# Optimization experiments

Measured on AMD Instinct MI355X. Metric: run time of the kernel, lower is better.

Reference implementation:

```python
import jax, jax.numpy as jnp
import numpy as np

K = 16

def _local_cov(points):
    # points: [B, N, 3]. FoldingNet-style local covariance feature.
    xx = jnp.sum(points * points, axis=-1)                       # [B,N]
    inner = jnp.einsum('bnd,bmd->bnm', points, points)           # [B,N,N]
    pd = -xx[:, :, None] + 2.0 * inner - xx[:, None, :]          # negative sq dist
    _, idx = jax.lax.top_k(pd, K)                                # [B,N,K] nearest first (self at 0)
    n0 = jnp.take_along_axis(points, idx[:, :, 0][:, :, None], axis=1)  # [B,N,3]
    n1 = jnp.take_along_axis(points, idx[:, :, 1][:, :, None], axis=1)  # [B,N,3]
    cov = n0[..., :, None] * n1[..., None, :]                    # [B,N,3,3] outer product
    B, N = points.shape[0], points.shape[1]
    return jnp.concatenate([points, cov.reshape(B, N, 9)], axis=-1)     # [B,N,12]

def _stage(x, w1, b1, wr, br, w2, b2):
    h = jax.nn.relu(x @ w1 + b1)
    h = jax.nn.relu(h + (h @ wr + br))   # ResidualLinearLayer then ReLU
    return h @ w2 + b2                   # [B,N,1]

def setup_inputs() -> dict:
    key = jax.random.key(0)
    ks = jax.random.split(key, 16)
    B, N, F = 8, 4096, 512
    s = 0.02
    d = {
        'latent': jax.random.normal(ks[0], (B, N, F), jnp.float32),
        'reconstructed_points': jax.random.normal(ks[1], (B, 3, N), jnp.float32),
        's1_w1': jax.random.normal(ks[2], (F + 12, F), jnp.float32) * s,
        's1_b1': jnp.zeros((F,), jnp.float32),
        's1_wr': jax.random.normal(ks[3], (F, F), jnp.float32) * s,
        's1_br': jnp.zeros((F,), jnp.float32),
        's1_w2': jax.random.normal(ks[4], (F, 1), jnp.float32) * s,
        's1_b2': jnp.zeros((1,), jnp.float32),
        's2_w1': jax.random.normal(ks[5], (F + 1, F), jnp.float32) * s,
        's2_b1': jnp.zeros((F,), jnp.float32),
        's2_wr': jax.random.normal(ks[6], (F, F), jnp.float32) * s,
        's2_br': jnp.zeros((F,), jnp.float32),
        's2_w2': jax.random.normal(ks[7], (F, 1), jnp.float32) * s,
        's2_b2': jnp.zeros((1,), jnp.float32),
        's3_w1': jax.random.normal(ks[8], (F + 1, F), jnp.float32) * s,
        's3_b1': jnp.zeros((F,), jnp.float32),
        's3_wr': jax.random.normal(ks[9], (F, F), jnp.float32) * s,
        's3_br': jnp.zeros((F,), jnp.float32),
        's3_w2': jax.random.normal(ks[10], (F, 1), jnp.float32) * s,
        's3_b2': jnp.zeros((1,), jnp.float32),
    }
    return d

def reference(latent, reconstructed_points,
              s1_w1, s1_b1, s1_wr, s1_br, s1_w2, s1_b2,
              s2_w1, s2_b1, s2_wr, s2_br, s2_w2, s2_b2,
              s3_w1, s3_b1, s3_wr, s3_br, s3_w2, s3_b2):
    pts = jnp.transpose(reconstructed_points, (0, 2, 1))   # [B,N,3]
    local = _local_cov(pts)                                 # [B,N,12]
    f1 = jnp.concatenate([latent, local], axis=-1)
    std1 = _stage(f1, s1_w1, s1_b1, s1_wr, s1_br, s1_w2, s1_b2)
    f2 = jnp.concatenate([latent, std1], axis=-1)
    std2 = std1 + _stage(f2, s2_w1, s2_b1, s2_wr, s2_br, s2_w2, s2_b2)
    f3 = jnp.concatenate([latent, std2], axis=-1)
    std3 = std2 + _stage(f3, s3_w1, s3_b1, s3_wr, s3_br, s3_w2, s3_b2)
    return std3   # [B,N,1]
```

## Files before the change

### kernel.cpp

```cpp
#include <hip/hip_runtime.h>

typedef __bf16 bf16x8 __attribute__((ext_vector_type(8)));
typedef float f32x4 __attribute__((ext_vector_type(4)));

__device__ __forceinline__ unsigned short f2bf(float f) {
  unsigned u = __float_as_uint(f);
  u += 0x7FFFu + ((u >> 16) & 1u);
  return (unsigned short)(u >> 16);
}

__device__ __forceinline__ void gload_lds16(const void* g, void* l) {
  __builtin_amdgcn_global_load_lds((const __attribute__((address_space(1))) void*)g,
                                   (__attribute__((address_space(3))) void*)l,
                                   16, 0, 0);
}

#define NPTS 4096
#define LDX 576

__global__ __launch_bounds__(256) void convw6_kernel(
    const float* w0, const float* w1, const float* w2,
    const float* r0, const float* r1, const float* r2,
    unsigned short* d0, unsigned short* d1, unsigned short* d2,
    unsigned short* e0, unsigned short* e1, unsigned short* e2) {
  int z = blockIdx.z;
  const float* src; unsigned short* dst; int Ksrc, Kpad, addI;
  switch (z) {
    case 0: src = w0; dst = d0; Ksrc = 524; Kpad = 576; addI = 0; break;
    case 1: src = w1; dst = d1; Ksrc = 513; Kpad = 576; addI = 0; break;
    case 2: src = w2; dst = d2; Ksrc = 513; Kpad = 576; addI = 0; break;
    case 3: src = r0; dst = e0; Ksrc = 512; Kpad = 512; addI = 1; break;
    case 4: src = r1; dst = e1; Ksrc = 512; Kpad = 512; addI = 1; break;
    default: src = r2; dst = e2; Ksrc = 512; Kpad = 512; addI = 1; break;
  }
  int k0 = blockIdx.x * 32;
  if (k0 >= Kpad) return;
  __shared__ float tile[32][33];
  int n0 = blockIdx.y * 32;
  int tx = threadIdx.x & 31, ty = threadIdx.x >> 5;
#pragma unroll
  for (int r = 0; r < 32; r += 8) {
    int k = k0 + ty + r, n = n0 + tx;
    tile[ty + r][tx] = (k < Ksrc) ? src[(size_t)k * 512 + n] : 0.f;
  }
  __syncthreads();
#pragma unroll
  for (int r = 0; r < 32; r += 8) {
    int n = n0 + ty + r, k = k0 + tx;
    float v = tile[tx][ty + r];
    if (addI && n == k) v += 1.0f;
    dst[(size_t)n * Kpad + k] = f2bf(v);
  }
}

__global__ __launch_bounds__(256) void conv_latent_kernel(const float* __restrict__ latent,
                                                          unsigned short* __restrict__ X) {
  size_t idx = (size_t)blockIdx.x * 256 + threadIdx.x;
  size_t m = idx >> 7;
  int c4 = (int)(idx & 127) * 4;
  float4 v = *(const float4*)(latent + m * 512 + c4);
  ushort4 o;
  o.x = f2bf(v.x); o.y = f2bf(v.y); o.z = f2bf(v.z); o.w = f2bf(v.w);
  *(ushort4*)(X + m * LDX + c4) = o;
}

__device__ __forceinline__ void merge2(float& v1, int& i1, float& v2, int& i2, int mk) {
  float ov1 = __shfl_xor(v1, mk); int oi1 = __shfl_xor(i1, mk);
  float ov2 = __shfl_xor(v2, mk); int oi2 = __shfl_xor(i2, mk);
  bool ofirst = (ov1 > v1) || (ov1 == v1 && oi1 < i1);
  float n1v, n2v; int n1i, n2i;
  if (ofirst) {
    n1v = ov1; n1i = oi1;
    bool t = (v1 > ov2) || (v1 == ov2 && i1 < oi2);
    n2v = t ? v1 : ov2; n2i = t ? i1 : oi2;
  } else {
    n1v = v1; n1i = i1;
    bool t = (ov1 > v2) || (ov1 == v2 && oi1 < i2);
    n2v = t ? ov1 : v2; n2i = t ? oi1 : i2;
  }
  v1 = n1v; i1 = n1i; v2 = n2v; i2 = n2i;
}

__global__ __launch_bounds__(512) void knn_kernel(const float* __restrict__ rp,
                                                  unsigned short* __restrict__ X) {
  __shared__ float4 P[NPTS];
  int b = blockIdx.y;
  const float* base = rp + (size_t)b * 3 * NPTS;
  for (int j = threadIdx.x; j < NPTS; j += 512) {
    float x = base[j], y = base[NPTS + j], z = base[2 * NPTS + j];
    float xx = __fadd_rn(__fadd_rn(__fmul_rn(x, x), __fmul_rn(y, y)), __fmul_rn(z, z));
    P[j] = make_float4(x, y, z, xx);
  }
  __syncthreads();
  int wave = threadIdx.x >> 6, lane = threadIdx.x & 63;
  int grp = lane >> 4, slice = lane & 15;
  int il0 = wave * 16 + grp * 4;
  int ibase = blockIdx.x * 128 + il0;
  float tx[4], ty[4], tz[4], tc[4];
  float v1[4], v2[4]; int i1[4], i2[4];
#pragma unroll
  for (int p = 0; p < 4; ++p) {
    float4 pp = P[ibase + p];
    tx[p] = 2.f * pp.x; ty[p] = 2.f * pp.y; tz[p] = 2.f * pp.z; tc[p] = -pp.w;
    v1[p] = -3.4e38f; v2[p] = -3.4e38f; i1[p] = 0x7fffffff; i2[p] = 0x7fffffff;
  }
#pragma unroll 4
  for (int t = 0; t < NPTS / 16; ++t) {
    int j = t * 16 + slice;
    float4 pj = P[j];
#pragma unroll
    for (int p = 0; p < 4; ++p) {
      float d = __builtin_fmaf(tx[p], pj.x,
                __builtin_fmaf(ty[p], pj.y,
                __builtin_fmaf(tz[p], pj.z, tc[p]))) - pj.w;
      bool c1 = d > v1[p];
      bool c2 = d > v2[p];
      i2[p] = c1 ? i1[p] : (c2 ? j : i2[p]);
      v2[p] = __builtin_amdgcn_fmed3f(d, v1[p], v2[p]);
      i1[p] = c1 ? j : i1[p];
      v1[p] = fmaxf(v1[p], d);
    }
  }
#pragma unroll
  for (int mk = 1; mk <= 8; mk <<= 1)
#pragma unroll
    for (int p = 0; p < 4; ++p)
      merge2(v1[p], i1[p], v2[p], i2[p], mk);
  if (slice == 0) {
#pragma unroll
    for (int p = 0; p < 4; ++p) {
      float4 p0 = P[i1[p]];
      float4 p1 = P[i2[p]];
      size_t row = (size_t)b * NPTS + ibase + p;
      unsigned short* xp = X + row * LDX + 512;
      float px = 0.5f * tx[p], py = 0.5f * ty[p], pz = 0.5f * tz[p];
      float vals[12] = { px, py, pz,
                         p0.x * p1.x, p0.x * p1.y, p0.x * p1.z,
                         p0.y * p1.x, p0.y * p1.y, p0.y * p1.z,
                         p0.z * p1.x, p0.z * p1.y, p0.z * p1.z };
#pragma unroll
      for (int k = 0; k < 12; ++k) xp[k] = f2bf(vals[k]);
#pragma unroll
      for (int k = 12; k < 32; ++k) xp[k] = 0;
    }
  }
}

#define BM 128
#define BN 128
#define BK 64
__global__ __launch_bounds__(256) void gemm_relu_kernel(
    const unsigned short* __restrict__ Xb, const unsigned short* __restrict__ Wt,
    const float* __restrict__ bias, unsigned short* __restrict__ H,
    int K, int ldx, int ldw) {
  __shared__ unsigned short As[BM * BK];
  __shared__ unsigned short Bs[BN * BK];
  const int t = threadIdx.x;
  const int wave = t >> 6, lane = t & 63;
  const int m0 = blockIdx.y * BM, n0 = blockIdx.x * BN;
  const int wm = (wave >> 1) * 64, wn = (wave & 1) * 64;
  const int sr = lane >> 2;
  const int sc = (lane & 3) * 8;
  const int q = lane >> 4, lm = lane & 15;
  f32x4 acc[4][4] = {};
  for (int kt = 0; kt < K; kt += BK) {
#pragma unroll
    for (int r = 0; r < 2; ++r) {
      int c = r * 4 + wave;
#pragma unroll
      for (int h = 0; h < 2; ++h) {
        gload_lds16(Xb + (size_t)(m0 + c * 16 + sr) * ldx + kt + h * 32 + sc,
                    As + c * 1024 + h * 512);
        gload_lds16(Wt + (size_t)(n0 + c * 16 + sr) * ldw + kt + h * 32 + sc,
                    Bs + c * 1024 + h * 512);
      }
    }
    __syncthreads();
#pragma unroll
    for (int ks = 0; ks < 2; ++ks) {
      bf16x8 a[4], bb[4];
#pragma unroll
      for (int i = 0; i < 4; ++i)
        a[i] = *(const bf16x8*)(As + ((wm >> 4) + i) * 1024 + ks * 512 + lm * 32 + q * 8);
#pragma unroll
      for (int j = 0; j < 4; ++j)
        bb[j] = *(const bf16x8*)(Bs + ((wn >> 4) + j) * 1024 + ks * 512 + lm * 32 + q * 8);
#pragma unroll
      for (int i = 0; i < 4; ++i)
#pragma unroll
        for (int j = 0; j < 4; ++j)
          acc[i][j] = __builtin_amdgcn_mfma_f32_16x16x32_bf16(a[i], bb[j], acc[i][j], 0, 0, 0);
    }
    __syncthreads();
  }
#pragma unroll
  for (int i = 0; i < 4; ++i)
#pragma unroll
    for (int j = 0; j < 4; ++j) {
      int col = n0 + wn + j * 16 + lm;
      float bv = bias[col];
#pragma unroll
      for (int rg = 0; rg < 4; ++rg) {
        int row = m0 + wm + i * 16 + q * 4 + rg;
        float v = acc[i][j][rg] + bv;
        v = v > 0.f ? v : 0.f;
        H[(size_t)row * 512 + col] = f2bf(v);
      }
    }
}

__global__ __launch_bounds__(256) void gemm_res_kernel(
    const unsigned short* __restrict__ H1, const unsigned short* __restrict__ Wt,
    const float* __restrict__ br, const float* __restrict__ w2,
    float* __restrict__ so) {
  __shared__ unsigned short As[BM * BK];
  __shared__ unsigned short Bs[BN * BK];
  const int t = threadIdx.x;
  const int wave = t >> 6, lane = t & 63;
  const int m0 = blockIdx.y * BM, n0 = blockIdx.x * BN;
  const int wm = (wave >> 1) * 64, wn = (wave & 1) * 64;
  const int sr = lane >> 2, sc = (lane & 3) * 8;
  const int q = lane >> 4, lm = lane & 15;
  f32x4 acc[4][4] = {};
  for (int kt = 0; kt < 512; kt += BK) {
#pragma unroll
    for (int r = 0; r < 2; ++r) {
      int c = r * 4 + wave;
#pragma unroll
      for (int h = 0; h < 2; ++h) {
        gload_lds16(H1 + (size_t)(m0 + c * 16 + sr) * 512 + kt + h * 32 + sc,
                    As + c * 1024 + h * 512);
        gload_lds16(Wt + (size_t)(n0 + c * 16 + sr) * 512 + kt + h * 32 + sc,
                    Bs + c * 1024 + h * 512);
      }
    }
    __syncthreads();
#pragma unroll
    for (int ks = 0; ks < 2; ++ks) {
      bf16x8 a[4], bb[4];
#pragma unroll
      for (int i = 0; i < 4; ++i)
        a[i] = *(const bf16x8*)(As + ((wm >> 4) + i) * 1024 + ks * 512 + lm * 32 + q * 8);
#pragma unroll
      for (int j = 0; j < 4; ++j)
        bb[j] = *(const bf16x8*)(Bs + ((wn >> 4) + j) * 1024 + ks * 512 + lm * 32 + q * 8);
#pragma unroll
      for (int i = 0; i < 4; ++i)
#pragma unroll
        for (int j = 0; j < 4; ++j)
          acc[i][j] = __builtin_amdgcn_mfma_f32_16x16x32_bf16(a[i], bb[j], acc[i][j], 0, 0, 0);
    }
    __syncthreads();
  }
  float partial[4][4];
#pragma unroll
  for (int i = 0; i < 4; ++i)
#pragma unroll
    for (int rg = 0; rg < 4; ++rg) partial[i][rg] = 0.f;
#pragma unroll
  for (int i = 0; i < 4; ++i)
#pragma unroll
    for (int j = 0; j < 4; ++j) {
      int col = n0 + wn + j * 16 + lm;
      float bv = br[col], wv = w2[col];
#pragma unroll
      for (int rg = 0; rg < 4; ++rg) {
        float v = acc[i][j][rg] + bv;
        v = v > 0.f ? v : 0.f;
        partial[i][rg] += v * wv;
      }
    }
#pragma unroll
  for (int i = 0; i < 4; ++i)
#pragma unroll
    for (int rg = 0; rg < 4; ++rg) {
      float s = partial[i][rg];
      s += __shfl_xor(s, 1); s += __shfl_xor(s, 2);
      s += __shfl_xor(s, 4); s += __shfl_xor(s, 8);
      if (lm == 0) atomicAdd(&so[m0 + wm + i * 16 + q * 4 + rg], s);
    }
}

__global__ __launch_bounds__(256) void init_so_kernel(float* so, const float* b2) {
  int m = blockIdx.x * 256 + threadIdx.x;
  so[m] = b2[0];
}
__global__ __launch_bounds__(256) void update_kernel(float* std_cum, float* so,
                                                     unsigned short* X,
                                                     const float* b2_next, int first) {
  int m = blockIdx.x * 256 + threadIdx.x;
  float s = so[m];
  if (!first) s += std_cum[m];
  std_cum[m] = s;
  unsigned short* xp = X + (size_t)m * LDX + 512;
  xp[0] = f2bf(s);
#pragma unroll
  for (int k = 1; k < 12; ++k) xp[k] = 0;
  so[m] = b2_next[0];
}
__global__ __launch_bounds__(256) void finalize_kernel(float* out, const float* std_cum,
                                                       const float* so) {
  int m = blockIdx.x * 256 + threadIdx.x;
  out[m] = std_cum[m] + so[m];
}

extern "C" void kernel_launch(void* const* d_in, const int* in_sizes, int n_in,
                              void* d_out, int out_size, void* d_ws, size_t ws_size,
                              hipStream_t stream) {
  const int B = 8, N = NPTS, M = B * N;
  const float* latent = (const float*)d_in[0];
  const float* rp = (const float*)d_in[1];
  const float* w1[3] = {(const float*)d_in[2], (const float*)d_in[8], (const float*)d_in[14]};
  const float* b1[3] = {(const float*)d_in[3], (const float*)d_in[9], (const float*)d_in[15]};
  const float* wr[3] = {(const float*)d_in[4], (const float*)d_in[10], (const float*)d_in[16]};
  const float* br[3] = {(const float*)d_in[5], (const float*)d_in[11], (const float*)d_in[17]};
  const float* w2[3] = {(const float*)d_in[6], (const float*)d_in[12], (const float*)d_in[18]};
  const float* b2[3] = {(const float*)d_in[7], (const float*)d_in[13], (const float*)d_in[19]};

  char* ws = (char*)d_ws;
  auto carve = [&](size_t bytes) {
    char* p = ws;
    ws += (bytes + 255) & ~(size_t)255;
    return p;
  };
  unsigned short* X  = (unsigned short*)carve((size_t)M * LDX * 2);
  unsigned short* H1 = (unsigned short*)carve((size_t)M * 512 * 2);
  unsigned short* W1t[3], *Wrt[3];
  for (int s = 0; s < 3; ++s) W1t[s] = (unsigned short*)carve((size_t)512 * LDX * 2);
  for (int s = 0; s < 3; ++s) Wrt[s] = (unsigned short*)carve((size_t)512 * 512 * 2);
  float* std_cum = (float*)carve((size_t)M * 4);
  float* so      = (float*)carve((size_t)M * 4);

  convw6_kernel<<<dim3(LDX / 32, 16, 6), 256, 0, stream>>>(
      w1[0], w1[1], w1[2], wr[0], wr[1], wr[2],
      W1t[0], W1t[1], W1t[2], Wrt[0], Wrt[1], Wrt[2]);
  conv_latent_kernel<<<(M * 128) / 256, 256, 0, stream>>>(latent, X);
  knn_kernel<<<dim3(N / 128, B), 512, 0, stream>>>(rp, X);
  init_so_kernel<<<M / 256, 256, 0, stream>>>(so, b2[0]);

  for (int s = 0; s < 3; ++s) {
    gemm_relu_kernel<<<dim3(4, M / BM), 256, 0, stream>>>(X, W1t[s], b1[s], H1, LDX, LDX, LDX);
    gemm_res_kernel<<<dim3(4, M / BM), 256, 0, stream>>>(H1, Wrt[s], br[s], w2[s], so);
    if (s < 2)
      update_kernel<<<M / 256, 256, 0, stream>>>(std_cum, so, X, b2[s + 1], s == 0 ? 1 : 0);
  }
  finalize_kernel<<<M / 256, 256, 0, stream>>>((float*)d_out, std_cum, so);
}
```

Before: 400.0 us.

## Use 32x32 MFMA tiles in GEMMs and simplify kNN to nearest non-self

```diff
diff --git a/kernel.cpp b/kernel.cpp
--- a/kernel.cpp
+++ b/kernel.cpp
@@ -1,7 +1,7 @@
 #include <hip/hip_runtime.h>
 
 typedef __bf16 bf16x8 __attribute__((ext_vector_type(8)));
-typedef float f32x4 __attribute__((ext_vector_type(4)));
+typedef float f32x16 __attribute__((ext_vector_type(16)));
 
 __device__ __forceinline__ unsigned short f2bf(float f) {
   unsigned u = __float_as_uint(f);
@@ -64,21 +64,10 @@
   *(ushort4*)(X + m * LDX + c4) = o;
 }
 
-__device__ __forceinline__ void merge2(float& v1, int& i1, float& v2, int& i2, int mk) {
-  float ov1 = __shfl_xor(v1, mk); int oi1 = __shfl_xor(i1, mk);
-  float ov2 = __shfl_xor(v2, mk); int oi2 = __shfl_xor(i2, mk);
-  bool ofirst = (ov1 > v1) || (ov1 == v1 && oi1 < i1);
-  float n1v, n2v; int n1i, n2i;
-  if (ofirst) {
-    n1v = ov1; n1i = oi1;
-    bool t = (v1 > ov2) || (v1 == ov2 && i1 < oi2);
-    n2v = t ? v1 : ov2; n2i = t ? i1 : oi2;
-  } else {
-    n1v = v1; n1i = i1;
-    bool t = (ov1 > v2) || (ov1 == v2 && oi1 < i2);
-    n2v = t ? ov1 : v2; n2i = t ? oi1 : i2;
-  }
-  v1 = n1v; i1 = n1i; v2 = n2v; i2 = n2i;
+__device__ __forceinline__ void merge1(float& v, int& j, int mk) {
+  float ov = __shfl_xor(v, mk); int oj = __shfl_xor(j, mk);
+  bool take = (ov > v) || (ov == v && oj < j);
+  v = take ? ov : v; j = take ? oj : j;
 }
 
 __global__ __launch_bounds__(512) void knn_kernel(const float* __restrict__ rp,
@@ -89,55 +78,51 @@
   for (int j = threadIdx.x; j < NPTS; j += 512) {
     float x = base[j], y = base[NPTS + j], z = base[2 * NPTS + j];
     float xx = __fadd_rn(__fadd_rn(__fmul_rn(x, x), __fmul_rn(y, y)), __fmul_rn(z, z));
-    P[j] = make_float4(x, y, z, xx);
+    P[j] = make_float4(x, y, z, -xx);
   }
   __syncthreads();
   int wave = threadIdx.x >> 6, lane = threadIdx.x & 63;
   int grp = lane >> 4, slice = lane & 15;
-  int il0 = wave * 16 + grp * 4;
-  int ibase = blockIdx.x * 128 + il0;
-  float tx[4], ty[4], tz[4], tc[4];
-  float v1[4], v2[4]; int i1[4], i2[4];
-#pragma unroll
-  for (int p = 0; p < 4; ++p) {
-    float4 pp = P[ibase + p];
-    tx[p] = 2.f * pp.x; ty[p] = 2.f * pp.y; tz[p] = 2.f * pp.z; tc[p] = -pp.w;
-    v1[p] = -3.4e38f; v2[p] = -3.4e38f; i1[p] = 0x7fffffff; i2[p] = 0x7fffffff;
-  }
-#pragma unroll 4
+  int il0 = wave * 8 + grp * 2;
+  int ia = blockIdx.x * 64 + il0;
+  int ib = ia + 1;
+  float4 pa = P[ia], pb = P[ib];
+  float ax = 2.f * pa.x, ay = 2.f * pa.y, az = 2.f * pa.z;
+  float bx = 2.f * pb.x, by = 2.f * pb.y, bz = 2.f * pb.z;
+  float va = -3.4e38f, vb = -3.4e38f;
+  int ta = 0, tb = 0;
+  int sta = ((ia & 15) == slice) ? (ia >> 4) : -1;
+  int stb = ((ib & 15) == slice) ? (ib >> 4) : -1;
+  const float4* pp = P + slice;
+#pragma unroll 8
   for (int t = 0; t < NPTS / 16; ++t) {
-    int j = t * 16 + slice;
-    float4 pj = P[j];
-#pragma unroll
-    for (int p = 0; p < 4; ++p) {
-      float d = __builtin_fmaf(tx[p], pj.x,
-                __builtin_fmaf(ty[p], pj.y,
-                __builtin_fmaf(tz[p], pj.z, tc[p]))) - pj.w;
-      bool c1 = d > v1[p];
-      bool c2 = d > v2[p];
-      i2[p] = c1 ? i1[p] : (c2 ? j : i2[p]);
-      v2[p] = __builtin_amdgcn_fmed3f(d, v1[p], v2[p]);
-      i1[p] = c1 ? j : i1[p];
-      v1[p] = fmaxf(v1[p], d);
-    }
-  }
-#pragma unroll
-  for (int mk = 1; mk <= 8; mk <<= 1)
-#pragma unroll
-    for (int p = 0; p < 4; ++p)
-      merge2(v1[p], i1[p], v2[p], i2[p], mk);
+    float4 pj = pp[t * 16];
+    float ea = __builtin_fmaf(ax, pj.x, __builtin_fmaf(ay, pj.y,
+               __builtin_fmaf(az, pj.z, pj.w)));
+    float eb = __builtin_fmaf(bx, pj.x, __builtin_fmaf(by, pj.y,
+               __builtin_fmaf(bz, pj.z, pj.w)));
+    ea = (t == sta) ? -3.4e38f : ea;
+    eb = (t == stb) ? -3.4e38f : eb;
+    bool ca = ea > va; va = ca ? ea : va; ta = ca ? t : ta;
+    bool cb = eb > vb; vb = cb ? eb : vb; tb = cb ? t : tb;
+  }
+  int ja = ta * 16 + slice, jb = tb * 16 + slice;
+#pragma unroll
+  for (int mk = 1; mk <= 8; mk <<= 1) {
+    merge1(va, ja, mk);
+    merge1(vb, jb, mk);
+  }
   if (slice == 0) {
 #pragma unroll
-    for (int p = 0; p < 4; ++p) {
-      float4 p0 = P[i1[p]];
-      float4 p1 = P[i2[p]];
-      size_t row = (size_t)b * NPTS + ibase + p;
+    for (int p = 0; p < 2; ++p) {
+      float4 pi = (p == 0) ? pa : pb;
+      float4 p1 = P[(p == 0) ? ja : jb];
+      size_t row = (size_t)b * NPTS + ia + p;
       unsigned short* xp = X + row * LDX + 512;
-      float px = 0.5f * tx[p], py = 0.5f * ty[p], pz = 0.5f * tz[p];
-      float vals[12] = { px, py, pz,
-                         p0.x * p1.x, p0.x * p1.y, p0.x * p1.z,
-                         p0.y * p1.x, p0.y * p1.y, p0.y * p1.z,
-                         p0.z * p1.x, p0.z * p1.y, p0.z * p1.z };
+      float vals[12] = { pi.x, pi.y, pi.z,
+                         pi.x * p1.x, pi.x * p1.y, pi.x * p1.z,
+                         pi.y * p1.x, pi.y * p1.y, pi.y * p1.z,
+                         pi.z * p1.x, pi.z * p1.y, pi.z * p1.z };
 #pragma unroll
       for (int k = 0; k < 12; ++k) xp[k] = f2bf(vals[k]);
 #pragma unroll
@@ -159,10 +144,9 @@
   const int wave = t >> 6, lane = t & 63;
   const int m0 = blockIdx.y * BM, n0 = blockIdx.x * BN;
   const int wm = (wave >> 1) * 64, wn = (wave & 1) * 64;
-  const int sr = lane >> 2;
-  const int sc = (lane & 3) * 8;
-  const int q = lane >> 4, lm = lane & 15;
-  f32x4 acc[4][4] = {};
+  const int sr = lane >> 2, sc = (lane & 3) * 8;
+  const int l31 = lane & 31, hi = lane >> 5;
+  f32x16 acc[2][2] = {};
   for (int kt = 0; kt < K; kt += BK) {
 #pragma unroll
     for (int r = 0; r < 2; ++r) {
@@ -177,36 +161,43 @@
     }
     __syncthreads();
 #pragma unroll
-    for (int ks = 0; ks < 2; ++ks) {
-      bf16x8 a[4], bb[4];
-#pragma unroll
-      for (int i = 0; i < 4; ++i)
-        a[i] = *(const bf16x8*)(As + ((wm >> 4) + i) * 1024 + ks * 512 + lm * 32 + q * 8);
-#pragma unroll
-      for (int j = 0; j < 4; ++j)
-        bb[j] = *(const bf16x8*)(Bs + ((wn >> 4) + j) * 1024 + ks * 512 + lm * 32 + q * 8);
-#pragma unroll
-      for (int i = 0; i < 4; ++i)
-#pragma unroll
-        for (int j = 0; j < 4; ++j)
-          acc[i][j] = __builtin_amdgcn_mfma_f32_16x16x32_bf16(a[i], bb[j], acc[i][j], 0, 0, 0);
+    for (int ks = 0; ks < 4; ++ks) {
+      bf16x8 a[2], bb[2];
+#pragma unroll
+      for (int i = 0; i < 2; ++i) {
+        int rt = wm + i * 32 + l31;
+        a[i] = *(const bf16x8*)(As + (rt >> 4) * 1024 + (ks >> 1) * 512 +
+                                (rt & 15) * 32 + (ks & 1) * 16 + hi * 8);
+      }
+#pragma unroll
+      for (int j = 0; j < 2; ++j) {
+        int rt = wn + j * 32 + l31;
+        bb[j] = *(const bf16x8*)(Bs + (rt >> 4) * 1024 + (ks >> 1) * 512 +
+                                 (rt & 15) * 32 + (ks & 1) * 16 + hi * 8);
+      }
+#pragma unroll
+      for (int i = 0; i < 2; ++i)
+#pragma unroll
+        for (int j = 0; j < 2; ++j)
+          acc[i][j] = __builtin_amdgcn_mfma_f32_32x32x16_bf16(a[i], bb[j], acc[i][j], 0, 0, 0);
     }
     __syncthreads();
   }
 #pragma unroll
-  for (int i = 0; i < 4; ++i)
-#pragma unroll
-    for (int j = 0; j < 4; ++j) {
-      int col = n0 + wn + j * 16 + lm;
-      float bv = bias[col];
-#pragma unroll
-      for (int rg = 0; rg < 4; ++rg) {
-        int row = m0 + wm + i * 16 + q * 4 + rg;
+  for (int j = 0; j < 2; ++j) {
+    int col = n0 + wn + j * 32 + l31;
+    float bv = bias[col];
+#pragma unroll
+    for (int i = 0; i < 2; ++i) {
+#pragma unroll
+      for (int rg = 0; rg < 16; ++rg) {
+        int row = m0 + wm + i * 32 + (rg & 3) + 8 * (rg >> 2) + 4 * hi;
         float v = acc[i][j][rg] + bv;
         v = v > 0.f ? v : 0.f;
         H[(size_t)row * 512 + col] = f2bf(v);
       }
     }
+  }
 }
 
 __global__ __launch_bounds__(256) void gemm_res_kernel(
@@ -220,8 +211,8 @@
   const int m0 = blockIdx.y * BM, n0 = blockIdx.x * BN;
   const int wm = (wave >> 1) * 64, wn = (wave & 1) * 64;
   const int sr = lane >> 2, sc = (lane & 3) * 8;
-  const int q = lane >> 4, lm = lane & 15;
-  f32x4 acc[4][4] = {};
+  const int l31 = lane & 31, hi = lane >> 5;
+  f32x16 acc[2][2] = {};
   for (int kt = 0; kt < 512; kt += BK) {
 #pragma unroll
     for (int r = 0; r < 2; ++r) {
@@ -236,48 +227,57 @@
     }
     __syncthreads();
 #pragma unroll
-    for (int ks = 0; ks < 2; ++ks) {
-      bf16x8 a[4], bb[4];
-#pragma unroll
-      for (int i = 0; i < 4; ++i)
-        a[i] = *(const bf16x8*)(As + ((wm >> 4) + i) * 1024 + ks * 512 + lm * 32 + q * 8);
-#pragma unroll
-      for (int j = 0; j < 4; ++j)
-        bb[j] = *(const bf16x8*)(Bs + ((wn >> 4) + j) * 1024 + ks * 512 + lm * 32 + q * 8);
-#pragma unroll
-      for (int i = 0; i < 4; ++i)
-#pragma unroll
-        for (int j = 0; j < 4; ++j)
-          acc[i][j] = __builtin_amdgcn_mfma_f32_16x16x32_bf16(a[i], bb[j], acc[i][j], 0, 0, 0);
+    for (int ks = 0; ks < 4; ++ks) {
+      bf16x8 a[2], bb[2];
+#pragma unroll
+      for (int i = 0; i < 2; ++i) {
+        int rt = wm + i * 32 + l31;
+        a[i] = *(const bf16x8*)(As + (rt >> 4) * 1024 + (ks >> 1) * 512 +
+                                (rt & 15) * 32 + (ks & 1) * 16 + hi * 8);
+      }
+#pragma unroll
+      for (int j = 0; j < 2; ++j) {
+        int rt = wn + j * 32 + l31;
+        bb[j] = *(const bf16x8*)(Bs + (rt >> 4) * 1024 + (ks >> 1) * 512 +
+                                 (rt & 15) * 32 + (ks & 1) * 16 + hi * 8);
+      }
+#pragma unroll
+      for (int i = 0; i < 2; ++i)
+#pragma unroll
+        for (int j = 0; j < 2; ++j)
+          acc[i][j] = __builtin_amdgcn_mfma_f32_32x32x16_bf16(a[i], bb[j], acc[i][j], 0, 0, 0);
     }
     __syncthreads();
   }
-  float partial[4][4];
-#pragma unroll
-  for (int i = 0; i < 4; ++i)
-#pragma unroll
-    for (int rg = 0; rg < 4; ++rg) partial[i][rg] = 0.f;
-#pragma unroll
-  for (int i = 0; i < 4; ++i)
-#pragma unroll
-    for (int j = 0; j < 4; ++j) {
-      int col = n0 + wn + j * 16 + lm;
-      float bv = br[col], wv = w2[col];
-#pragma unroll
-      for (int rg = 0; rg < 4; ++rg) {
+  float pr[2][16];
+#pragma unroll
+  for (int i = 0; i < 2; ++i)
+#pragma unroll
+    for (int rg = 0; rg < 16; ++rg) pr[i][rg] = 0.f;
+#pragma unroll
+  for (int j = 0; j < 2; ++j) {
+    int col = n0 + wn + j * 32 + l31;
+    float bv = br[col], wv = w2[col];
+#pragma unroll
+    for (int i = 0; i < 2; ++i)
+#pragma unroll
+      for (int rg = 0; rg < 16; ++rg) {
         float v = acc[i][j][rg] + bv;
         v = v > 0.f ? v : 0.f;
-        partial[i][rg] += v * wv;
-      }
-    }
-#pragma unroll
-  for (int i = 0; i < 4; ++i)
-#pragma unroll
-    for (int rg = 0; rg < 4; ++rg) {
-      float s = partial[i][rg];
-      s += __shfl_xor(s, 1); s += __shfl_xor(s, 2);
-      s += __shfl_xor(s, 4); s += __shfl_xor(s, 8);
-      if (lm == 0) atomicAdd(&so[m0 + wm + i * 16 + q * 4 + rg], s);
+        pr[i][rg] += v * wv;
+      }
+  }
+#pragma unroll
+  for (int i = 0; i < 2; ++i)
+#pragma unroll
+    for (int rg = 0; rg < 16; ++rg) {
+      float s = pr[i][rg];
+      s += __shfl_xor(s, 1); s += __shfl_xor(s, 2); s += __shfl_xor(s, 4);
+      s += __shfl_xor(s, 8); s += __shfl_xor(s, 16);
+      if (l31 == 0) {
+        int row = m0 + wm + i * 32 + (rg & 3) + 8 * (rg >> 2) + 4 * hi;
+        atomicAdd(&so[row], s);
+      }
     }
 }
 
@@ -335,7 +335,7 @@
       w1[0], w1[1], w1[2], wr[0], wr[1], wr[2],
       W1t[0], W1t[1], W1t[2], Wrt[0], Wrt[1], Wrt[2]);
   conv_latent_kernel<<<(M * 128) / 256, 256, 0, stream>>>(latent, X);
-  knn_kernel<<<dim3(N / 128, B), 512, 0, stream>>>(rp, X);
+  knn_kernel<<<dim3(N / 64, B), 512, 0, stream>>>(rp, X);
   init_so_kernel<<<M / 256, 256, 0, stream>>>(so, b2[0]);
 
   for (int s = 0; s < 3; ++s) {
```

After: 413.5 us. 3.4% more time.
